# Kernel optimization log

Hardware: AMD Instinct MI355X
Metric: run time of the kernel (lower is better)

## Reference

```python
import jax, jax.numpy as jnp
import numpy as np

B, S, V, D, H, T = 16, 256, 32000, 512, 512, 50


def setup_inputs() -> dict:
    key = jax.random.key(0)
    ks = jax.random.split(key, 6)
    tokens = jax.random.randint(ks[0], (B, S), 0, V, dtype=jnp.int64)
    topic_probs = jax.random.uniform(ks[1], (B, S, T), dtype=jnp.float32)
    topic_probs = topic_probs / jnp.linalg.norm(topic_probs, axis=-1, keepdims=True)
    embed_table = jax.random.normal(ks[2], (V, D), dtype=jnp.float32) * 0.02
    lstm_kernel = jax.random.normal(ks[3], (T + D + H, 4 * H), dtype=jnp.float32) * 0.02
    lstm_bias = jnp.zeros((4 * H,), dtype=jnp.float32)
    dense_w = jax.random.normal(ks[4], (H, V), dtype=jnp.float32) * 0.02
    dense_b = jnp.zeros((V,), dtype=jnp.float32)
    return {"tokens": tokens, "topic_probs": topic_probs, "embed_table": embed_table,
            "lstm_kernel": lstm_kernel, "lstm_bias": lstm_bias,
            "dense_w": dense_w, "dense_b": dense_b}


def _lstm(xs, kernel, bias):
    # xs: [B, S, T+D]; TF LSTMCell gate order: i, j(cell cand), f, o; forget_bias=0.0
    h_dim = bias.shape[0] // 4
    b = xs.shape[0]

    def step(carry, xt):
        c, h = carry
        z = jnp.concatenate([xt, h], axis=-1) @ kernel + bias  # [B, 4H]
        i, j, f, o = jnp.split(z, 4, axis=-1)
        c = jax.nn.sigmoid(f) * c + jax.nn.sigmoid(i) * jnp.tanh(j)
        h = jax.nn.sigmoid(o) * jnp.tanh(c)
        return (c, h), h

    init = (jnp.zeros((b, h_dim), xs.dtype), jnp.zeros((b, h_dim), xs.dtype))
    _, hs = jax.lax.scan(step, init, jnp.swapaxes(xs, 0, 1))  # [S, B, H]
    return jnp.swapaxes(hs, 0, 1)


def reference(tokens, topic_probs, embed_table, lstm_kernel, lstm_bias, dense_w, dense_b):
    word_emb = embed_table[tokens]                         # [B, S, D]
    xs = jnp.concatenate([topic_probs, word_emb], axis=-1)  # [B, S, T+D]
    hs = _lstm(xs, lstm_kernel, lstm_bias)                 # [B, S, H]
    logits = hs @ dense_w + dense_b                        # [B, S, V]
    return logits
```

## Files before the change

kernel.cpp:

```cpp
#include <hip/hip_runtime.h>
#include <cstdint>
#include <cstddef>

#define B_ 16
#define S_ 256
#define V_ 32000
#define D_ 512
#define H_ 512
#define T_ 50
#define KX (T_ + D_)
#define KXP 576
#define G4 (4 * H_)
#define M_ (B_ * S_)

#define GBLK 64
#define NWRK 192
#define UPB 8
#define WST 512
#define NJT 16
#define NNT 250

typedef unsigned short u16;
typedef unsigned int u32;
typedef __attribute__((ext_vector_type(8))) short bf16x8;
typedef __attribute__((ext_vector_type(4))) float f32x4;
typedef __attribute__((ext_vector_type(4))) u16 u16x4;
typedef __attribute__((ext_vector_type(8))) u16 u16x8;
typedef __attribute__((ext_vector_type(4))) u32 u32x4;

__device__ __forceinline__ float sigmoidf_(float x) { return 1.f / (1.f + expf(-x)); }

__device__ __forceinline__ u16 f2bf_rne(float x) {
  u32 u = __float_as_uint(x);
  u32 r = (u + 0x7fffu + ((u >> 16) & 1u)) >> 16;
  return (u16)r;
}
__device__ __forceinline__ float bf2f(u16 h) { return __uint_as_float(((u32)h) << 16); }

__device__ __forceinline__ int swz(int row, int k) {
  return row * WST + (k ^ ((row & 7) << 3));
}

#define GLD_LDS16(g, l) __builtin_amdgcn_global_load_lds( \
    (const __attribute__((address_space(1))) void*)(g), \
    (__attribute__((address_space(3))) void*)(l), 16, 0, 0)

__global__ __launch_bounds__(256) void gather_split_x(
    const int* __restrict__ tokens, const float* __restrict__ topic,
    const float* __restrict__ embed, u16* __restrict__ Xhi,
    u16* __restrict__ Xlo) {
  const int m = blockIdx.x;
  const int tok = tokens[m];
  const int k4 = threadIdx.x * 4;
  if (k4 >= KXP) return;
  u16x4 hv, lv;
  #pragma unroll
  for (int i = 0; i < 4; ++i) {
    int k = k4 + i;
    float v = 0.f;
    if (k < T_)       v = topic[(size_t)m * T_ + k];
    else if (k < KX)  v = embed[(size_t)tok * D_ + (k - T_)];
    u16 h = f2bf_rne(v);
    hv[i] = h;
    lv[i] = f2bf_rne(v - bf2f(h));
  }
  size_t o = (size_t)m * KXP + k4;
  *(u16x4*)(Xhi + o) = hv;
  *(u16x4*)(Xlo + o) = lv;
}

__global__ __launch_bounds__(256) void wx_split_t(
    const float* __restrict__ W, u16* __restrict__ Whi, u16* __restrict__ Wlo) {
  __shared__ float tile[32][33];
  const int n0 = blockIdx.x * 32, k0 = blockIdx.y * 32;
  const int r = threadIdx.x >> 3;
  const int c4 = (threadIdx.x & 7) * 4;
  const int kg = k0 + r;
  const float* src = W + (size_t)kg * G4 + n0 + c4;
  #pragma unroll
  for (int i = 0; i < 4; ++i) tile[r][c4 + i] = (kg < KX) ? src[i] : 0.f;
  __syncthreads();
  u16x4 hv, lv;
  #pragma unroll
  for (int i = 0; i < 4; ++i) {
    float x = tile[c4 + i][r];
    u16 h = f2bf_rne(x);
    hv[i] = h;
    lv[i] = f2bf_rne(x - bf2f(h));
  }
  size_t o = (size_t)(n0 + r) * KXP + k0 + c4;
  *(u16x4*)(Whi + o) = hv;
  *(u16x4*)(Wlo + o) = lv;
}

__global__ __launch_bounds__(256) void proj_mfma(
    const u16* __restrict__ Ahi, const u16* __restrict__ Alo,
    const u16* __restrict__ Bhi, const u16* __restrict__ Blo,
    const float* __restrict__ bias, float* __restrict__ C) {
  __shared__ u16 lds[4][128 * 32];
  const int tid = threadIdx.x;
  const int w = tid >> 6, lane = tid & 63;
  const int bm = blockIdx.y * 128;
  const int bn = blockIdx.x * 128;
  const int wm = (w >> 1) * 64, wn = (w & 1) * 64;

  f32x4 acc[4][4];
  #pragma unroll
  for (int m = 0; m < 4; ++m)
    #pragma unroll
    for (int n = 0; n < 4; ++n) acc[m][n] = (f32x4){0.f, 0.f, 0.f, 0.f};

  const u16* src0 = Ahi + (size_t)bm * KXP;
  const u16* src1 = Alo + (size_t)bm * KXP;
  const u16* src2 = Bhi + (size_t)bn * KXP;
  const u16* src3 = Blo + (size_t)bn * KXP;

  const int lrow = lane >> 2;
  const int lkb  = (lane & 3) * 8;
  const int kb   = (lane >> 4) * 8;

  for (int k0 = 0; k0 < KXP; k0 += 32) {
    #pragma unroll
    for (int cc = 0; cc < 2; ++cc) {
      const int c = w * 2 + cc;
      const int row = c * 16 + lrow;
      const size_t goff = (size_t)row * KXP + k0 + lkb;
      u16* l = &lds[0][0] + c * 16 * 32;
      GLD_LDS16(src0 + goff, l);
      GLD_LDS16(src1 + goff, l + 128 * 32);
      GLD_LDS16(src2 + goff, l + 2 * 128 * 32);
      GLD_LDS16(src3 + goff, l + 3 * 128 * 32);
    }
    __syncthreads();

    bf16x8 ah[4], al[4], bh[4], bl[4];
    #pragma unroll
    for (int m = 0; m < 4; ++m) {
      int r = wm + m * 16 + (lane & 15);
      ah[m] = *(const bf16x8*)&lds[0][r * 32 + kb];
      al[m] = *(const bf16x8*)&lds[1][r * 32 + kb];
    }
    #pragma unroll
    for (int n = 0; n < 4; ++n) {
      int r = wn + n * 16 + (lane & 15);
      bh[n] = *(const bf16x8*)&lds[2][r * 32 + kb];
      bl[n] = *(const bf16x8*)&lds[3][r * 32 + kb];
    }
    #pragma unroll
    for (int m = 0; m < 4; ++m)
      #pragma unroll
      for (int n = 0; n < 4; ++n) {
        acc[m][n] = __builtin_amdgcn_mfma_f32_16x16x32_bf16(al[m], bh[n], acc[m][n], 0, 0, 0);
        acc[m][n] = __builtin_amdgcn_mfma_f32_16x16x32_bf16(ah[m], bl[n], acc[m][n], 0, 0, 0);
        acc[m][n] = __builtin_amdgcn_mfma_f32_16x16x32_bf16(ah[m], bh[n], acc[m][n], 0, 0, 0);
      }
    __syncthreads();
  }

  const int lc = lane & 15, lr4 = (lane >> 4) * 4;
  #pragma unroll
  for (int n = 0; n < 4; ++n) {
    int col = bn + wn + n * 16 + lc;
    float bv = bias[col];
    #pragma unroll
    for (int m = 0; m < 4; ++m) {
      int row0 = bm + wm + m * 16 + lr4;
      float* Cp = C + (size_t)row0 * G4 + col;
      #pragma unroll
      for (int j = 0; j < 4; ++j)
        Cp[(size_t)j * G4] = acc[m][n][j] + bv;
    }
  }
}

__global__ __launch_bounds__(256) void split_w_t(
    const float* __restrict__ W, u16* __restrict__ Whi, u16* __restrict__ Wlo) {
  __shared__ float tile[32][33];
  const int n0 = blockIdx.x * 32, k0 = blockIdx.y * 32;
  const int r = threadIdx.x >> 3;
  const int c4 = (threadIdx.x & 7) * 4;
  const float* src = W + (size_t)(k0 + r) * V_ + n0 + c4;
  #pragma unroll
  for (int i = 0; i < 4; ++i) tile[r][c4 + i] = src[i];
  __syncthreads();
  u16x4 hv, lv;
  #pragma unroll
  for (int i = 0; i < 4; ++i) {
    float x = tile[c4 + i][r];
    u16 h = f2bf_rne(x);
    hv[i] = h;
    lv[i] = f2bf_rne(x - bf2f(h));
  }
  size_t o = (size_t)(n0 + r) * 512 + k0 + c4;
  *(u16x4*)(Whi + o) = hv;
  *(u16x4*)(Wlo + o) = lv;
}

__global__ __launch_bounds__(256, 1) void fused_lstm_dense(
    const float* __restrict__ xs_proj, const float* __restrict__ Wh,
    u32* __restrict__ hpk,
    u32* __restrict__ Apk,
    u32* __restrict__ ctr,
    const u16* __restrict__ Bhi, const u16* __restrict__ Blo,
    const float* __restrict__ bias, float* __restrict__ out) {
  __shared__ u16 whi_l[32 * WST];
  __shared__ u16 wlo_l[32 * WST];
  __shared__ u16 hhi_l[16 * WST];
  __shared__ u16 hlo_l[16 * WST];
  __shared__ float zpart[4][16][34];
  __shared__ u16 Ah_l[256 * 32];
  __shared__ u16 Al_l[256 * 32];
  __shared__ u16 Bh_l[128 * 32];
  __shared__ u16 Bl_l[128 * 32];

  const int bid = blockIdx.x;
  const int tid = threadIdx.x;
  const int w = tid >> 6;
  const int lane = tid & 63;

  if (bid < GBLK) {
    const int u0 = bid * UPB;

    for (int idx = tid; idx < 32 * 512; idx += 256) {
      int c = idx & 31, k = idx >> 5;
      int gc = (c >> 3) * 512 + u0 + (c & 7);
      float v = Wh[(size_t)k * G4 + gc];
      u16 hi = f2bf_rne(v);
      int si = swz(c, k);
      whi_l[si] = hi;
      wlo_l[si] = f2bf_rne(v - bf2f(hi));
    }

    float c_reg = 0.f;
    const int rb = tid >> 3;
    const int rj = tid & 7;
    const int kb = (lane >> 4) * 8;
    const int l15 = lane & 15;

    for (int s = 0; s < S_; ++s) {
      float zi = 0.f, zj2 = 0.f, zf = 0.f, zo = 0.f;
      if (tid < 128) {
        const float* zp = xs_proj + ((size_t)rb * S_ + s) * G4 + u0 + rj;
        zi = zp[0]; zj2 = zp[512]; zf = zp[1024]; zo = zp[1536];
      }

      if (s > 0) {
        if (tid == 0) {
          const u32 tgt = 64u * (u32)s;
          while (__hip_atomic_load(ctr, __ATOMIC_RELAXED,
                                   __HIP_MEMORY_SCOPE_AGENT) < tgt)
            __builtin_amdgcn_s_sleep(1);
        }
        __syncthreads();
        asm volatile("" ::: "memory");
      }

      {
        const u32* src = hpk + (size_t)(s & 1) * 8192;
        u32 v[32];
        #pragma unroll
        for (int j = 0; j < 32; ++j)
          v[j] = __hip_atomic_load(src + tid + j * 256, __ATOMIC_RELAXED,
                                   __HIP_MEMORY_SCOPE_AGENT);
        #pragma unroll
        for (int j = 0; j < 32; ++j) {
          int idx = tid + j * 256;
          int b = idx >> 9, u = idx & 511;
          int si = swz(b, u);
          hhi_l[si] = (u16)(v[j] & 0xffffu);
          hlo_l[si] = (u16)(v[j] >> 16);
        }
      }
      __syncthreads();

      {
        f32x4 acc0 = {0.f, 0.f, 0.f, 0.f};
        f32x4 acc1 = {0.f, 0.f, 0.f, 0.f};
        #pragma unroll
        for (int ks = 0; ks < 4; ++ks) {
          const int k = w * 128 + ks * 32 + kb;
          const int ia = swz(l15, k);
          const int ib = swz(16 + l15, k);
          bf16x8 ah  = *(const bf16x8*)&hhi_l[ia];
          bf16x8 al  = *(const bf16x8*)&hlo_l[ia];
          bf16x8 b0h = *(const bf16x8*)&whi_l[ia];
          bf16x8 b0l = *(const bf16x8*)&wlo_l[ia];
          bf16x8 b1h = *(const bf16x8*)&whi_l[ib];
          bf16x8 b1l = *(const bf16x8*)&wlo_l[ib];
          acc0 = __builtin_amdgcn_mfma_f32_16x16x32_bf16(al, b0h, acc0, 0, 0, 0);
          acc0 = __builtin_amdgcn_mfma_f32_16x16x32_bf16(ah, b0l, acc0, 0, 0, 0);
          acc0 = __builtin_amdgcn_mfma_f32_16x16x32_bf16(ah, b0h, acc0, 0, 0, 0);
          acc1 = __builtin_amdgcn_mfma_f32_16x16x32_bf16(al, b1h, acc1, 0, 0, 0);
          acc1 = __builtin_amdgcn_mfma_f32_16x16x32_bf16(ah, b1l, acc1, 0, 0, 0);
          acc1 = __builtin_amdgcn_mfma_f32_16x16x32_bf16(ah, b1h, acc1, 0, 0, 0);
        }
        #pragma unroll
        for (int jj = 0; jj < 4; ++jj) {
          int r = (lane >> 4) * 4 + jj;
          zpart[w][r][l15] = acc0[jj];
          zpart[w][r][16 + l15] = acc1[jj];
        }
      }
      __syncthreads();

      if (tid < 128) {
        #pragma unroll
        for (int ww = 0; ww < 4; ++ww) {
          zi  += zpart[ww][rb][rj];
          zj2 += zpart[ww][rb][8 + rj];
          zf  += zpart[ww][rb][16 + rj];
          zo  += zpart[ww][rb][24 + rj];
        }
        float cc = sigmoidf_(zf) * c_reg + sigmoidf_(zi) * tanhf(zj2);
        c_reg = cc;
        float h = sigmoidf_(zo) * tanhf(cc);
        u16 hh = f2bf_rne(h);
        u16 hl = f2bf_rne(h - bf2f(hh));
        u32 pack = (u32)hh | ((u32)hl << 16);
        const int hoff = rb * 512 + u0 + rj;
        __hip_atomic_store(hpk + (size_t)((s + 1) & 1) * 8192 + hoff, pack,
                           __ATOMIC_RELAXED, __HIP_MEMORY_SCOPE_AGENT);
        const size_t ar = ((size_t)s * 16 + rb) * 512 + u0 + rj;
        __hip_atomic_store(Apk + ar, pack,
                           __ATOMIC_RELAXED, __HIP_MEMORY_SCOPE_AGENT);
      }
      asm volatile("s_waitcnt vmcnt(0)" ::: "memory");
      __syncthreads();

      if (tid == 0)
        __hip_atomic_fetch_add(ctr, 1u, __ATOMIC_RELAXED,
                               __HIP_MEMORY_SCOPE_AGENT);
    }
  } else {
    const int wid = bid - GBLK;
    const int wm = (w >> 1) * 128, wn = (w & 1) * 64;
    const int l15 = lane & 15;
    const int kb = (lane >> 4) * 8;
    const int lrow = lane >> 2;
    const int lkb = (lane & 3) * 8;

    int lastj = -1;
    for (int t = wid; t < NJT * NNT; t += NWRK) {
      const int jt = t / NNT;
      const int n  = t - jt * NNT;
      if (jt != lastj) {
        if (tid == 0) {
          const u32 tgt = 1024u * (u32)(jt + 1);
          while (__hip_atomic_load(ctr, __ATOMIC_RELAXED,
                                   __HIP_MEMORY_SCOPE_AGENT) < tgt)
            __builtin_amdgcn_s_sleep(32);
        }
        __syncthreads();
        asm volatile("" ::: "memory");
        lastj = jt;
      }

      const int bmA = jt * 256;
      const int bn = n * 128;
      f32x4 acc[8][4];
      #pragma unroll
      for (int m = 0; m < 8; ++m)
        #pragma unroll
        for (int q = 0; q < 4; ++q) acc[m][q] = (f32x4){0.f, 0.f, 0.f, 0.f};

      const u16* srcBh = Bhi + (size_t)bn * 512;
      const u16* srcBl = Blo + (size_t)bn * 512;

      for (int k0 = 0; k0 < 512; k0 += 32) {
        {
          const u32* ap = Apk + (size_t)(bmA + tid) * 512 + k0;
          u32x4 a[8];
          #pragma unroll
          for (int i = 0; i < 8; ++i) a[i] = *(const u32x4*)(ap + i * 4);
          #pragma unroll
          for (int g = 0; g < 4; ++g) {
            u16x8 hv, lv;
            #pragma unroll
            for (int i = 0; i < 4; ++i) {
              hv[i]     = (u16)(a[2*g][i] & 0xffffu);
              lv[i]     = (u16)(a[2*g][i] >> 16);
              hv[4 + i] = (u16)(a[2*g+1][i] & 0xffffu);
              lv[4 + i] = (u16)(a[2*g+1][i] >> 16);
            }
            *(u16x8*)&Ah_l[tid * 32 + g * 8] = hv;
            *(u16x8*)&Al_l[tid * 32 + g * 8] = lv;
          }
        }
        #pragma unroll
        for (int cc = 0; cc < 2; ++cc) {
          const int c = w * 2 + cc;
          const int row = c * 16 + lrow;
          const size_t goff = (size_t)row * 512 + k0 + lkb;
          GLD_LDS16(srcBh + goff, &Bh_l[c * 16 * 32]);
          GLD_LDS16(srcBl + goff, &Bl_l[c * 16 * 32]);
        }
        __syncthreads();

        bf16x8 bh[4], bl[4];
        #pragma unroll
        for (int q = 0; q < 4; ++q) {
          int r = wn + q * 16 + l15;
          bh[q] = *(const bf16x8*)&Bh_l[r * 32 + kb];
          bl[q] = *(const bf16x8*)&Bl_l[r * 32 + kb];
        }
        #pragma unroll
        for (int m = 0; m < 8; ++m) {
          int r = wm + m * 16 + l15;
          bf16x8 ah = *(const bf16x8*)&Ah_l[r * 32 + kb];
          bf16x8 al = *(const bf16x8*)&Al_l[r * 32 + kb];
          #pragma unroll
          for (int q = 0; q < 4; ++q) {
            acc[m][q] = __builtin_amdgcn_mfma_f32_16x16x32_bf16(al, bh[q], acc[m][q], 0, 0, 0);
            acc[m][q] = __builtin_amdgcn_mfma_f32_16x16x32_bf16(ah, bl[q], acc[m][q], 0, 0, 0);
            acc[m][q] = __builtin_amdgcn_mfma_f32_16x16x32_bf16(ah, bh[q], acc[m][q], 0, 0, 0);
          }
        }
        __syncthreads();
      }

      const int lc = lane & 15, lr4 = (lane >> 4) * 4;
      #pragma unroll
      for (int q = 0; q < 4; ++q) {
        int col = bn + wn + q * 16 + lc;
        float bv = bias[col];
        #pragma unroll
        for (int m = 0; m < 8; ++m) {
          int mbase = bmA + wm + m * 16;
          int s = mbase >> 4;
          float* Cp = out + ((size_t)lr4 * 256 + s) * V_ + col;
          #pragma unroll
          for (int jj = 0; jj < 4; ++jj)
            Cp[(size_t)jj * 256 * V_] = acc[m][q][jj] + bv;
        }
      }
    }
  }
}

extern "C" void kernel_launch(void* const* d_in, const int* in_sizes, int n_in,
                              void* d_out, int out_size, void* d_ws, size_t ws_size,
                              hipStream_t stream) {
  const int*   tokens = (const int*)  d_in[0];
  const float* topic  = (const float*)d_in[1];
  const float* embed  = (const float*)d_in[2];
  const float* lk     = (const float*)d_in[3];
  const float* lb     = (const float*)d_in[4];
  const float* dw     = (const float*)d_in[5];
  const float* db     = (const float*)d_in[6];
  float* out = (float*)d_out;

  char* ws = (char*)d_ws;
  size_t off = 0;
  float* xs_proj = (float*)(ws + off); off += (size_t)M_ * G4 * 4;
  char* xa = ws + off;
  u16* Xhi = (u16*)xa;
  u16* Xlo = (u16*)(xa + (size_t)M_ * KXP * 2);
  u32* Apk = (u32*)xa;
  off += (size_t)M_ * KXP * 2 * 2;
  u16* Whi = (u16*)(ws + off); off += (size_t)V_ * 512 * 2;
  u16* Wlo = (u16*)(ws + off); off += (size_t)V_ * 512 * 2;
  u16* Wxhi = (u16*)(ws + off); off += (size_t)G4 * KXP * 2;
  u16* Wxlo = (u16*)(ws + off); off += (size_t)G4 * KXP * 2;
  u32* hpk = (u32*)(ws + off); off += 2 * 8192 * 4;
  u32* ctr = (u32*)(ws + off); off += 256;

  hipMemsetAsync(hpk, 0, 2 * 8192 * 4, stream);
  hipMemsetAsync(ctr, 0, 256, stream);

  hipLaunchKernelGGL(split_w_t, dim3(V_ / 32, 512 / 32), dim3(256), 0, stream,
                     dw, Whi, Wlo);
  hipLaunchKernelGGL(wx_split_t, dim3(G4 / 32, KXP / 32), dim3(256), 0, stream,
                     lk, Wxhi, Wxlo);
  hipLaunchKernelGGL(gather_split_x, dim3(M_), dim3(256), 0, stream,
                     tokens, topic, embed, Xhi, Xlo);

  hipLaunchKernelGGL(proj_mfma, dim3(G4 / 128, M_ / 128), dim3(256), 0, stream,
                     Xhi, Xlo, Wxhi, Wxlo, lb, xs_proj);

  const float* Wh = lk + (size_t)KX * G4;
  hipLaunchKernelGGL(fused_lstm_dense, dim3(GBLK + NWRK), dim3(256), 0, stream,
                     xs_proj, Wh, hpk, Apk, ctr, Whi, Wlo, db, out);
}
```

Baseline: 1.219 ms.

## Double-buffer dense GEMM LDS tiles with prefetch, swizzle A layout, union shared memory

```diff
diff --git a/kernel.cpp b/kernel.cpp
--- a/kernel.cpp
+++ b/kernel.cpp
@@ -196,6 +196,22 @@
   *(u16x4*)(Wlo + o) = lv;
 }
 
+union SharedMem {
+  struct {
+    u16 whi[32 * WST];
+    u16 wlo[32 * WST];
+    u16 hhi[16 * WST];
+    u16 hlo[16 * WST];
+    float zpart[4][16][34];
+  } lstm;
+  struct {
+    u16 Ah[2][256 * 32];
+    u16 Al[2][256 * 32];
+    u16 Bh[2][128 * 32];
+    u16 Bl[2][128 * 32];
+  } dense;
+};
+
 __global__ __launch_bounds__(256, 1) void fused_lstm_dense(
     const float* __restrict__ xs_proj, const float* __restrict__ Wh,
     u32* __restrict__ hpk,
@@ -203,15 +219,7 @@
     u32* __restrict__ ctr,
     const u16* __restrict__ Bhi, const u16* __restrict__ Blo,
     const float* __restrict__ bias, float* __restrict__ out) {
-  __shared__ u16 whi_l[32 * WST];
-  __shared__ u16 wlo_l[32 * WST];
-  __shared__ u16 hhi_l[16 * WST];
-  __shared__ u16 hlo_l[16 * WST];
-  __shared__ float zpart[4][16][34];
-  __shared__ u16 Ah_l[256 * 32];
-  __shared__ u16 Al_l[256 * 32];
-  __shared__ u16 Bh_l[128 * 32];
-  __shared__ u16 Bl_l[128 * 32];
+  __shared__ SharedMem sm;
 
   const int bid = blockIdx.x;
   const int tid = threadIdx.x;
@@ -227,8 +235,8 @@
       float v = Wh[(size_t)k * G4 + gc];
       u16 hi = f2bf_rne(v);
       int si = swz(c, k);
-      whi_l[si] = hi;
-      wlo_l[si] = f2bf_rne(v - bf2f(hi));
+      sm.lstm.whi[si] = hi;
+      sm.lstm.wlo[si] = f2bf_rne(v - bf2f(hi));
     }
 
     float c_reg = 0.f;
@@ -267,8 +275,8 @@
           int idx = tid + j * 256;
           int b = idx >> 9, u = idx & 511;
           int si = swz(b, u);
-          hhi_l[si] = (u16)(v[j] & 0xffffu);
-          hlo_l[si] = (u16)(v[j] >> 16);
+          sm.lstm.hhi[si] = (u16)(v[j] & 0xffffu);
+          sm.lstm.hlo[si] = (u16)(v[j] >> 16);
         }
       }
       __syncthreads();
@@ -281,12 +289,12 @@
           const int k = w * 128 + ks * 32 + kb;
           const int ia = swz(l15, k);
           const int ib = swz(16 + l15, k);
-          bf16x8 ah  = *(const bf16x8*)&hhi_l[ia];
-          bf16x8 al  = *(const bf16x8*)&hlo_l[ia];
-          bf16x8 b0h = *(const bf16x8*)&whi_l[ia];
-          bf16x8 b0l = *(const bf16x8*)&wlo_l[ia];
-          bf16x8 b1h = *(const bf16x8*)&whi_l[ib];
-          bf16x8 b1l = *(const bf16x8*)&wlo_l[ib];
+          bf16x8 ah  = *(const bf16x8*)&sm.lstm.hhi[ia];
+          bf16x8 al  = *(const bf16x8*)&sm.lstm.hlo[ia];
+          bf16x8 b0h = *(const bf16x8*)&sm.lstm.whi[ia];
+          bf16x8 b0l = *(const bf16x8*)&sm.lstm.wlo[ia];
+          bf16x8 b1h = *(const bf16x8*)&sm.lstm.whi[ib];
+          bf16x8 b1l = *(const bf16x8*)&sm.lstm.wlo[ib];
           acc0 = __builtin_amdgcn_mfma_f32_16x16x32_bf16(al, b0h, acc0, 0, 0, 0);
           acc0 = __builtin_amdgcn_mfma_f32_16x16x32_bf16(ah, b0l, acc0, 0, 0, 0);
           acc0 = __builtin_amdgcn_mfma_f32_16x16x32_bf16(ah, b0h, acc0, 0, 0, 0);
@@ -297,8 +305,8 @@
         #pragma unroll
         for (int jj = 0; jj < 4; ++jj) {
           int r = (lane >> 4) * 4 + jj;
-          zpart[w][r][l15] = acc0[jj];
-          zpart[w][r][16 + l15] = acc1[jj];
+          sm.lstm.zpart[w][r][l15] = acc0[jj];
+          sm.lstm.zpart[w][r][16 + l15] = acc1[jj];
         }
       }
       __syncthreads();
@@ -306,10 +314,10 @@
       if (tid < 128) {
         #pragma unroll
         for (int ww = 0; ww < 4; ++ww) {
-          zi  += zpart[ww][rb][rj];
-          zj2 += zpart[ww][rb][8 + rj];
-          zf  += zpart[ww][rb][16 + rj];
-          zo  += zpart[ww][rb][24 + rj];
+          zi  += sm.lstm.zpart[ww][rb][rj];
+          zj2 += sm.lstm.zpart[ww][rb][8 + rj];
+          zf  += sm.lstm.zpart[ww][rb][16 + rj];
+          zo  += sm.lstm.zpart[ww][rb][24 + rj];
         }
         float cc = sigmoidf_(zf) * c_reg + sigmoidf_(zi) * tanhf(zj2);
         c_reg = cc;
@@ -338,6 +346,8 @@
     const int kb = (lane >> 4) * 8;
     const int lrow = lane >> 2;
     const int lkb = (lane & 3) * 8;
+    const int arow = tid >> 3;
+    const int acol = (tid & 7) * 4;
 
     int lastj = -1;
     for (int t = wid; t < NJT * NNT; t += NWRK) {
@@ -366,48 +376,68 @@
       const u16* srcBh = Bhi + (size_t)bn * 512;
       const u16* srcBl = Blo + (size_t)bn * 512;
 
-      for (int k0 = 0; k0 < 512; k0 += 32) {
-        {
-          const u32* ap = Apk + (size_t)(bmA + tid) * 512 + k0;
-          u32x4 a[8];
-          #pragma unroll
-          for (int i = 0; i < 8; ++i) a[i] = *(const u32x4*)(ap + i * 4);
-          #pragma unroll
-          for (int g = 0; g < 4; ++g) {
-            u16x8 hv, lv;
-            #pragma unroll
-            for (int i = 0; i < 4; ++i) {
-              hv[i]     = (u16)(a[2*g][i] & 0xffffu);
-              lv[i]     = (u16)(a[2*g][i] >> 16);
-              hv[4 + i] = (u16)(a[2*g+1][i] & 0xffffu);
-              lv[4 + i] = (u16)(a[2*g+1][i] >> 16);
-            }
-            *(u16x8*)&Ah_l[tid * 32 + g * 8] = hv;
-            *(u16x8*)&Al_l[tid * 32 + g * 8] = lv;
-          }
-        }
+      {
+        u32x4 a[8];
+        #pragma unroll
+        for (int i = 0; i < 8; ++i)
+          a[i] = *(const u32x4*)(Apk + (size_t)(bmA + i * 32 + arow) * 512 + acol);
         #pragma unroll
         for (int cc = 0; cc < 2; ++cc) {
           const int c = w * 2 + cc;
           const int row = c * 16 + lrow;
-          const size_t goff = (size_t)row * 512 + k0 + lkb;
-          GLD_LDS16(srcBh + goff, &Bh_l[c * 16 * 32]);
-          GLD_LDS16(srcBl + goff, &Bl_l[c * 16 * 32]);
+          const size_t goff = (size_t)row * 512 + lkb;
+          GLD_LDS16(srcBh + goff, &sm.dense.Bh[0][c * 16 * 32]);
+          GLD_LDS16(srcBl + goff, &sm.dense.Bl[0][c * 16 * 32]);
+        }
+        asm volatile("s_waitcnt vmcnt(0)" ::: "memory");
+        #pragma unroll
+        for (int i = 0; i < 8; ++i) {
+          const int row = i * 32 + arow;
+          u16x4 hv, lv;
+          #pragma unroll
+          for (int j = 0; j < 4; ++j) {
+            hv[j] = (u16)(a[i][j] & 0xffffu);
+            lv[j] = (u16)(a[i][j] >> 16);
+          }
+          const int col = acol ^ ((row & 3) << 3);
+          *(u16x4*)&sm.dense.Ah[0][row * 32 + col] = hv;
+          *(u16x4*)&sm.dense.Al[0][row * 32 + col] = lv;
         }
         __syncthreads();
+      }
+
+      int cur = 0;
+      for (int k0i = 0; k0i < 16; ++k0i) {
+        u32x4 a[8];
+        const int nxt = cur ^ 1;
+        if (k0i < 15) {
+          const int k0n = (k0i + 1) * 32;
+          #pragma unroll
+          for (int i = 0; i < 8; ++i)
+            a[i] = *(const u32x4*)(Apk + (size_t)(bmA + i * 32 + arow) * 512 + k0n + acol);
+          #pragma unroll
+          for (int cc = 0; cc < 2; ++cc) {
+            const int c = w * 2 + cc;
+            const int row = c * 16 + lrow;
+            const size_t goff = (size_t)row * 512 + k0n + lkb;
+            GLD_LDS16(srcBh + goff, &sm.dense.Bh[nxt][c * 16 * 32]);
+            GLD_LDS16(srcBl + goff, &sm.dense.Bl[nxt][c * 16 * 32]);
+          }
+        }
 
         bf16x8 bh[4], bl[4];
         #pragma unroll
         for (int q = 0; q < 4; ++q) {
           int r = wn + q * 16 + l15;
-          bh[q] = *(const bf16x8*)&Bh_l[r * 32 + kb];
-          bl[q] = *(const bf16x8*)&Bl_l[r * 32 + kb];
+          bh[q] = *(const bf16x8*)&sm.dense.Bh[cur][r * 32 + kb];
+          bl[q] = *(const bf16x8*)&sm.dense.Bl[cur][r * 32 + kb];
         }
         #pragma unroll
         for (int m = 0; m < 8; ++m) {
           int r = wm + m * 16 + l15;
-          bf16x8 ah = *(const bf16x8*)&Ah_l[r * 32 + kb];
-          bf16x8 al = *(const bf16x8*)&Al_l[r * 32 + kb];
+          int rcol = kb ^ ((r & 3) << 3);
+          bf16x8 ah = *(const bf16x8*)&sm.dense.Ah[cur][r * 32 + rcol];
+          bf16x8 al = *(const bf16x8*)&sm.dense.Al[cur][r * 32 + rcol];
           #pragma unroll
           for (int q = 0; q < 4; ++q) {
             acc[m][q] = __builtin_amdgcn_mfma_f32_16x16x32_bf16(al, bh[q], acc[m][q], 0, 0, 0);
@@ -415,7 +445,25 @@
             acc[m][q] = __builtin_amdgcn_mfma_f32_16x16x32_bf16(ah, bh[q], acc[m][q], 0, 0, 0);
           }
         }
+
+        if (k0i < 15) {
+          asm volatile("s_waitcnt vmcnt(0)" ::: "memory");
+          #pragma unroll
+          for (int i = 0; i < 8; ++i) {
+            const int row = i * 32 + arow;
+            u16x4 hv, lv;
+            #pragma unroll
+            for (int j = 0; j < 4; ++j) {
+              hv[j] = (u16)(a[i][j] & 0xffffu);
+              lv[j] = (u16)(a[i][j] >> 16);
+            }
+            const int col = acol ^ ((row & 3) << 3);
+            *(u16x4*)&sm.dense.Ah[nxt][row * 32 + col] = hv;
+            *(u16x4*)&sm.dense.Al[nxt][row * 32 + col] = lv;
+          }
+        }
         __syncthreads();
+        cur = nxt;
       }
 
       const int lc = lane & 15, lr4 = (lane >> 4) * 4;
```

Result: slower. 1.501 ms (+23.1%).
